# Kernel optimization log

Hardware: AMD Instinct MI355X
Metric: run time of the kernel (lower is better)

## Reference

```python
import jax, jax.numpy as jnp
import numpy as np

QLEN, B, D = 1024, 4, 512
H, DH = 8, 64
MEM, DMLP = 1024, 2048
KLEN = MEM + QLEN
EPS = 1e-5


def layer_norm(x, g, b):
    mu = jnp.mean(x, axis=-1, keepdims=True)
    var = jnp.var(x, axis=-1, keepdims=True)
    return (x - mu) * jax.lax.rsqrt(var + EPS) * g + b


def rel_shift(x):
    # x: [qlen, klen, b, h] -- Transformer-XL relative shift trick
    q, k, b, h = x.shape
    zp = jnp.zeros((q, 1, b, h), dtype=x.dtype)
    x = jnp.concatenate([zp, x], axis=1)          # [q, k+1, b, h]
    x = x.reshape(k + 1, q, b, h)[1:]             # drop first row
    return x.reshape(q, k, b, h)


def setup_inputs() -> dict:
    key = jax.random.key(0)
    ks = jax.random.split(key, 12)
    s = 0.02
    inp = {
        "inputs": jax.random.normal(ks[0], (QLEN, B, D), jnp.float32),
        "r": jax.random.normal(ks[1], (KLEN, D), jnp.float32),
        "u": jax.random.normal(ks[2], (H, DH), jnp.float32) * s,
        "v": jax.random.normal(ks[3], (H, DH), jnp.float32) * s,
        "mem": jax.random.normal(ks[4], (MEM, B, D), jnp.float32),
        # causal mask: query i (global pos MEM+i) cannot attend key j > MEM+i
        "attn_mask": jnp.arange(KLEN)[None, :] > (jnp.arange(QLEN)[:, None] + MEM),
        "Wqkv": jax.random.normal(ks[5], (3 * D, D), jnp.float32) * s,
        "Wr": jax.random.normal(ks[6], (D, D), jnp.float32) * s,
        "Wo": jax.random.normal(ks[7], (D, D), jnp.float32) * s,
        "ln1_g": jnp.ones((D,), jnp.float32),
        "ln1_b": jnp.zeros((D,), jnp.float32),
        "mlp_w1": jax.random.normal(ks[8], (DMLP, D), jnp.float32) * s,
        "mlp_b1": jnp.zeros((DMLP,), jnp.float32),
        "mlp_w2": jax.random.normal(ks[9], (D, DMLP), jnp.float32) * s,
        "mlp_b2": jnp.zeros((D,), jnp.float32),
        "ln2_g": jnp.ones((D,), jnp.float32),
        "ln2_b": jnp.zeros((D,), jnp.float32),
    }
    return inp


def reference(inputs, r, u, v, mem, attn_mask, Wqkv, Wr, Wo,
              ln1_g, ln1_b, mlp_w1, mlp_b1, mlp_w2, mlp_b2, ln2_g, ln2_b):
    qlen, b, d = inputs.shape
    cat = jnp.concatenate([mem, inputs], axis=0)          # [klen, b, d]
    klen = cat.shape[0]
    qkv = cat @ Wqkv.T                                    # [klen, b, 3d]
    q, k, w_v = jnp.split(qkv, 3, axis=-1)
    q = q[-qlen:].reshape(qlen, b, H, DH)
    k = k.reshape(klen, b, H, DH)
    w_v = w_v.reshape(klen, b, H, DH)
    rk = (r @ Wr.T).reshape(klen, H, DH)                  # [klen, h, dh]

    AC = jnp.einsum('ibhd,jbhd->ijbh', q + u, k)          # content term
    BD = jnp.einsum('ibhd,jhd->ijbh', q + v, rk)          # position term
    BD = rel_shift(BD)
    scale = 1.0 / np.sqrt(DH)
    score = (AC + BD) * scale                             # [q, k, b, h]
    score = jnp.where(attn_mask[:, :, None, None], jnp.float32(-1e30), score)
    prob = jax.nn.softmax(score, axis=1)
    attn = jnp.einsum('ijbh,jbhd->ibhd', prob, w_v).reshape(qlen, b, d)
    attn_out = attn @ Wo.T

    y = layer_norm(inputs + attn_out, ln1_g, ln1_b)
    h = jax.nn.relu(y @ mlp_w1.T + mlp_b1)
    z = h @ mlp_w2.T + mlp_b2
    out = layer_norm(y + z, ln2_g, ln2_b)
    return out, prob
```

## Files before the change

kernel.cpp:

```cpp
#include <hip/hip_runtime.h>
#include <math.h>

#define QL 1024
#define BSZ 4
#define DM 512
#define NH 8
#define DHH 64
#define MEML 1024
#define KL 2048
#define DMLP 2048

typedef __attribute__((ext_vector_type(8))) short bf16x8;
typedef __attribute__((ext_vector_type(4))) float f32x4;

#define MFMA16(A, B, C) __builtin_amdgcn_mfma_f32_16x16x32_bf16((A), (B), (C), 0, 0, 0)
#define SWZB(r, cb) (((r) << 7) + ((cb) ^ (((r) & 7) << 4)))
#define RINGB(r, c) (((r) << 9) + ((((c) << 2)) ^ (((r) & 7) << 4)))
#define CVT2(dst, lo, hi) \
  asm("v_cvt_pk_bf16_f32 %0, %1, %2" : "=v"(dst) : "v"(lo), "v"(hi))

__global__ __launch_bounds__(256)
void precvt_kernel(const float* __restrict__ src, unsigned short* __restrict__ hi,
                   unsigned short* __restrict__ lo, int n4) {
  const int i = blockIdx.x * 256 + threadIdx.x;
  if (i >= n4) return;
  const float4 a = ((const float4*)src)[i];
  uint2 h, l;
  CVT2(h.x, a.x, a.y); CVT2(h.y, a.z, a.w);
  float4 res;
  res.x = a.x - __uint_as_float(h.x << 16);
  res.y = a.y - __uint_as_float(h.x & 0xffff0000u);
  res.z = a.z - __uint_as_float(h.y << 16);
  res.w = a.w - __uint_as_float(h.y & 0xffff0000u);
  CVT2(l.x, res.x, res.y); CVT2(l.y, res.z, res.w);
  ((uint2*)hi)[i] = h;
  ((uint2*)lo)[i] = l;
}

template<int BM, bool APRE, bool BIAS, bool RELU>
__global__ __launch_bounds__(256)
void gemm_nt_mfma(const float* __restrict__ A0, const float* __restrict__ A1, int M0,
                  const unsigned short* __restrict__ AhiG, const unsigned short* __restrict__ AloG,
                  const unsigned short* __restrict__ WhiG, const unsigned short* __restrict__ WloG,
                  const float* __restrict__ bias,
                  float* __restrict__ C, int M, int N, int K) {
  constexpr int MR = 4;
  constexpr int NR = (BM == 128) ? 4 : 2;
  constexpr int AU = BM / 16;
  __shared__ __align__(16) unsigned short Ahi[BM * 64];
  __shared__ __align__(16) unsigned short Alo[BM * 64];
  __shared__ __align__(16) unsigned short Bhi[128 * 64];
  __shared__ __align__(16) unsigned short Blo[128 * 64];

  const int t = threadIdx.x;
  const int w = t >> 6;
  const int lane = t & 63;
  const int lq = lane & 15;
  const int lg = lane >> 4;
  const int row0 = blockIdx.y * BM, col0 = blockIdx.x * 128;
  const int wrow0 = (BM == 128) ? (w >> 1) * 64 : 0;
  const int wcol0 = (BM == 128) ? (w & 1) * 64 : w * 32;

  float4 paf[AU];
  uint2 pah[AU], pal[AU];
  uint2 pwh[8], pwl[8];

  auto loadAB = [&](int k0) {
    #pragma unroll
    for (int it = 0; it < AU; ++it) {
      const int idx = it * 256 + t;
      const int row = idx >> 4, c4 = (idx & 15) * 4;
      if (APRE) {
        const size_t off = (size_t)(row0 + row) * K + k0 + c4;
        pah[it] = *(const uint2*)(AhiG + off);
        pal[it] = *(const uint2*)(AloG + off);
      } else {
        const int grow = row0 + row;
        const float* src = (grow < M0) ? (A0 + (size_t)grow * K)
                                       : (A1 + (size_t)(grow - M0) * K);
        paf[it] = *(const float4*)(src + k0 + c4);
      }
    }
    #pragma unroll
    for (int it = 0; it < 8; ++it) {
      const int idx = it * 256 + t;
      const int row = idx >> 4, c4 = (idx & 15) * 4;
      const size_t off = (size_t)(col0 + row) * K + k0 + c4;
      pwh[it] = *(const uint2*)(WhiG + off);
      pwl[it] = *(const uint2*)(WloG + off);
    }
  };

  f32x4 acc[MR][NR];
  #pragma unroll
  for (int m = 0; m < MR; ++m)
    #pragma unroll
    for (int n = 0; n < NR; ++n)
      acc[m][n] = (f32x4){0.f, 0.f, 0.f, 0.f};

  loadAB(0);
  for (int k0 = 0; k0 < K; k0 += 64) {
    __syncthreads();
    #pragma unroll
    for (int it = 0; it < AU; ++it) {
      const int idx = it * 256 + t;
      const int row = idx >> 4, cb = (idx & 15) * 8;
      uint2 hi, lo;
      if (APRE) {
        hi = pah[it]; lo = pal[it];
      } else {
        const float4 a = paf[it];
        CVT2(hi.x, a.x, a.y); CVT2(hi.y, a.z, a.w);
        float4 res;
        res.x = a.x - __uint_as_float(hi.x << 16);
        res.y = a.y - __uint_as_float(hi.x & 0xffff0000u);
        res.z = a.z - __uint_as_float(hi.y << 16);
        res.w = a.w - __uint_as_float(hi.y & 0xffff0000u);
        CVT2(lo.x, res.x, res.y); CVT2(lo.y, res.z, res.w);
      }
      *(uint2*)((char*)Ahi + SWZB(row, cb)) = hi;
      *(uint2*)((char*)Alo + SWZB(row, cb)) = lo;
    }
    #pragma unroll
    for (int it = 0; it < 8; ++it) {
      const int idx = it * 256 + t;
      const int row = idx >> 4, cb = (idx & 15) * 8;
      *(uint2*)((char*)Bhi + SWZB(row, cb)) = pwh[it];
      *(uint2*)((char*)Blo + SWZB(row, cb)) = pwl[it];
    }
    __syncthreads();
    if (k0 + 64 < K) loadAB(k0 + 64);
    #pragma unroll
    for (int ks = 0; ks < 2; ++ks) {
      bf16x8 ah[MR], al[MR], bh[NR], bl[NR];
      #pragma unroll
      for (int m = 0; m < MR; ++m) {
        ah[m] = *(const bf16x8*)((const char*)Ahi + SWZB(wrow0 + m * 16 + lq, ks * 64 + lg * 16));
        al[m] = *(const bf16x8*)((const char*)Alo + SWZB(wrow0 + m * 16 + lq, ks * 64 + lg * 16));
      }
      #pragma unroll
      for (int n = 0; n < NR; ++n) {
        bh[n] = *(const bf16x8*)((const char*)Bhi + SWZB(wcol0 + n * 16 + lq, ks * 64 + lg * 16));
        bl[n] = *(const bf16x8*)((const char*)Blo + SWZB(wcol0 + n * 16 + lq, ks * 64 + lg * 16));
      }
      #pragma unroll
      for (int m = 0; m < MR; ++m)
        #pragma unroll
        for (int n = 0; n < NR; ++n) {
          acc[m][n] = MFMA16(ah[m], bh[n], acc[m][n]);
          acc[m][n] = MFMA16(ah[m], bl[n], acc[m][n]);
          acc[m][n] = MFMA16(al[m], bh[n], acc[m][n]);
        }
    }
  }
  #pragma unroll
  for (int n = 0; n < NR; ++n) {
    const int col = col0 + wcol0 + n * 16 + lq;
    const float bv = BIAS ? bias[col] : 0.f;
    #pragma unroll
    for (int m = 0; m < MR; ++m) {
      #pragma unroll
      for (int rg = 0; rg < 4; ++rg) {
        const int row = row0 + wrow0 + m * 16 + lg * 4 + rg;
        float vv = acc[m][n][rg] + bv;
        if (RELU) vv = fmaxf(vv, 0.f);
        C[(size_t)row * N + col] = vv;
      }
    }
  }
}

__global__ __launch_bounds__(256)
void ukvr_kernel(const float* __restrict__ QKV, const float* __restrict__ RK,
                 const float* __restrict__ u, const float* __restrict__ v,
                 float* __restrict__ UK, float* __restrict__ VR) {
  const int id = blockIdx.x * 256 + threadIdx.x;
  if (id < 65536) {
    const int bh = id >> 11, j = id & 2047;
    const int b = bh >> 3, h = bh & 7;
    const float* kp = QKV + ((size_t)j * 4 + b) * 1536 + 512 + h * 64;
    const float* up = u + h * 64;
    float s = 0.f;
    #pragma unroll
    for (int d = 0; d < 64; ++d) s += up[d] * kp[d];
    UK[id] = s;
  } else if (id < 65536 + 16384) {
    const int e = id - 65536;
    const int h = e >> 11, jr = e & 2047;
    const float* rp = RK + (size_t)jr * 512 + h * 64;
    const float* vp = v + h * 64;
    float s = 0.f;
    #pragma unroll
    for (int d = 0; d < 64; ++d) s += vp[d] * rp[d];
    VR[e] = s;
  }
}

__global__ __launch_bounds__(256)
void attn2_kernel(const float* __restrict__ QKV, const float* __restrict__ RK,
                  const float* __restrict__ UK, const float* __restrict__ VR,
                  unsigned short* __restrict__ P, float* __restrict__ INV,
                  float* __restrict__ ATTN) {
  const int b = blockIdx.y;
  const int h = blockIdx.z;
  const int i0 = (((h >> 2) & 1) ? (15 - (int)blockIdx.x) : (int)blockIdx.x) * 64;
  const int t = threadIdx.x;
  const int w = t >> 6;
  const int lane = t & 63;
  const int lq = lane & 15;
  const int lg = lane >> 4;

  __shared__ __align__(16) unsigned short Ks[4096];
  __shared__ __align__(16) unsigned short Rs[4096];
  __shared__ __align__(16) unsigned short Vt[4096];
  __shared__ __align__(16) unsigned short Es[4096];
  __shared__ __align__(16) float Ring[8192];
  __shared__ float uks[64];

  {
    const int jr0p = 960 - i0;
    #pragma unroll
    for (int it = 0; it < 4; ++it) {
      const int idx = it * 256 + t;
      const int row = idx >> 4, c4 = (idx & 15) * 4;
      const float4 q4 = *(const float4*)(QKV + ((size_t)(MEML + i0 + row) * 4 + b) * 1536 + h * 64 + c4);
      uint2 qp; CVT2(qp.x, q4.x, q4.y); CVT2(qp.y, q4.z, q4.w);
      *(uint2*)((char*)Es + SWZB(row, c4 * 2)) = qp;
      const float4 r4 = *(const float4*)(RK + (size_t)(jr0p + row) * 512 + h * 64 + c4);
      uint2 rp; CVT2(rp.x, r4.x, r4.y); CVT2(rp.y, r4.z, r4.w);
      *(uint2*)((char*)Rs + SWZB(row, c4 * 2)) = rp;
    }
  }
  __syncthreads();

  float4 pk[4], pr[4], pvv[4];
  float puk;
  auto load_tile = [&](int n) {
    const int j0 = n * 64;
    const int jr0 = j0 - i0 + 1024;
    #pragma unroll
    for (int it = 0; it < 4; ++it) {
      const int idx = it * 256 + t;
      const int row = idx >> 4, c4 = (idx & 15) * 4;
      pk[it] = *(const float4*)(QKV + ((size_t)(j0 + row) * 4 + b) * 1536 + 512 + h * 64 + c4);
      const int jr = jr0 + row;
      float4 r4 = make_float4(0.f, 0.f, 0.f, 0.f);
      if (jr < 2048) r4 = *(const float4*)(RK + (size_t)jr * 512 + h * 64 + c4);
      pr[it] = r4;
    }
    const int jb = (t >> 4) * 4, db = (t & 15) * 4;
    const float* vb = QKV + ((size_t)(j0 + jb) * 4 + b) * 1536 + 1024 + h * 64 + db;
    pvv[0] = *(const float4*)(vb);
    pvv[1] = *(const float4*)(vb + 6144);
    pvv[2] = *(const float4*)(vb + 12288);
    pvv[3] = *(const float4*)(vb + 18432);
    puk = (t < 64) ? UK[(size_t)(b * 8 + h) * 2048 + j0 + t] : 0.f;
  };
  load_tile(0);

  const bf16x8 qf0 = *(const bf16x8*)((const char*)Es + SWZB(w * 16 + lq, lg * 16));
  const bf16x8 qf1 = *(const bf16x8*)((const char*)Es + SWZB(w * 16 + lq, 64 + lg * 16));

  {
    f32x4 zero = {0.f, 0.f, 0.f, 0.f};
    f32x4 bd[4];
    #pragma unroll
    for (int nj = 0; nj < 4; ++nj) bd[nj] = zero;
    #pragma unroll
    for (int nj = 0; nj < 4; ++nj) {
      const bf16x8 rf0 = *(const bf16x8*)((const char*)Rs + SWZB(nj * 16 + lq, lg * 16));
      const bf16x8 rf1 = *(const bf16x8*)((const char*)Rs + SWZB(nj * 16 + lq, 64 + lg * 16));
      bd[nj] = MFMA16(qf0, rf0, bd[nj]);
      bd[nj] = MFMA16(qf1, rf1, bd[nj]);
    }
    const int jr0p = 960 - i0;
    #pragma unroll
    for (int nj = 0; nj < 4; ++nj) {
      const int jrl = nj * 16 + lq;
      const float vrv = VR[h * 2048 + jr0p + jrl];
      #pragma unroll
      for (int rg = 0; rg < 4; ++rg) {
        const int il = w * 16 + lg * 4 + rg;
        *(float*)((char*)Ring + RINGB(il, 64 + jrl)) = bd[nj][rg] + vrv;
      }
    }
  }

  f32x4 pv[4];
  {
    f32x4 zero = {0.f, 0.f, 0.f, 0.f};
    #pragma unroll
    for (int nd = 0; nd < 4; ++nd) pv[nd] = zero;
  }
  float rs[4] = {0.f, 0.f, 0.f, 0.f};

  const int ntiles = i0 / 64 + 17;
  for (int n = 0; n < ntiles; ++n) {
    const int j0 = n * 64;
    const int jr0 = j0 - i0 + 1024;
    __syncthreads();
    #pragma unroll
    for (int it = 0; it < 4; ++it) {
      const int idx = it * 256 + t;
      const int row = idx >> 4, c4 = (idx & 15) * 4;
      uint2 kp; CVT2(kp.x, pk[it].x, pk[it].y); CVT2(kp.y, pk[it].z, pk[it].w);
      *(uint2*)((char*)Ks + SWZB(row, c4 * 2)) = kp;
      uint2 rp; CVT2(rp.x, pr[it].x, pr[it].y); CVT2(rp.y, pr[it].z, pr[it].w);
      *(uint2*)((char*)Rs + SWZB(row, c4 * 2)) = rp;
    }
    {
      const int jb = (t >> 4) * 4, db = (t & 15) * 4;
      uint2 wv;
      CVT2(wv.x, pvv[0].x, pvv[1].x); CVT2(wv.y, pvv[2].x, pvv[3].x);
      *(uint2*)((char*)Vt + SWZB(db + 0, jb * 2)) = wv;
      CVT2(wv.x, pvv[0].y, pvv[1].y); CVT2(wv.y, pvv[2].y, pvv[3].y);
      *(uint2*)((char*)Vt + SWZB(db + 1, jb * 2)) = wv;
      CVT2(wv.x, pvv[0].z, pvv[1].z); CVT2(wv.y, pvv[2].z, pvv[3].z);
      *(uint2*)((char*)Vt + SWZB(db + 2, jb * 2)) = wv;
      CVT2(wv.x, pvv[0].w, pvv[1].w); CVT2(wv.y, pvv[2].w, pvv[3].w);
      *(uint2*)((char*)Vt + SWZB(db + 3, jb * 2)) = wv;
    }
    if (t < 64) uks[t] = puk;
    __syncthreads();
    if (n + 1 < ntiles) load_tile(n + 1);
    f32x4 acc[4], bdn[4];
    {
      f32x4 zero = {0.f, 0.f, 0.f, 0.f};
      #pragma unroll
      for (int nj = 0; nj < 4; ++nj) { acc[nj] = zero; bdn[nj] = zero; }
    }
    #pragma unroll
    for (int nj = 0; nj < 4; ++nj) {
      const bf16x8 kf0 = *(const bf16x8*)((const char*)Ks + SWZB(nj * 16 + lq, lg * 16));
      const bf16x8 rf0 = *(const bf16x8*)((const char*)Rs + SWZB(nj * 16 + lq, lg * 16));
      acc[nj] = MFMA16(qf0, kf0, acc[nj]);
      bdn[nj] = MFMA16(qf0, rf0, bdn[nj]);
      const bf16x8 kf1 = *(const bf16x8*)((const char*)Ks + SWZB(nj * 16 + lq, 64 + lg * 16));
      const bf16x8 rf1 = *(const bf16x8*)((const char*)Rs + SWZB(nj * 16 + lq, 64 + lg * 16));
      acc[nj] = MFMA16(qf1, kf1, acc[nj]);
      bdn[nj] = MFMA16(qf1, rf1, bdn[nj]);
    }
    const int base_cur = (n & 1) * 64;
    const int base_prev = 64 - base_cur;
    #pragma unroll
    for (int nj = 0; nj < 4; ++nj) {
      const int jrl = nj * 16 + lq;
      const int jrg = jr0 + jrl;
      const float vrv = (jrg < 2048) ? VR[h * 2048 + jrg] : 0.f;
      #pragma unroll
      for (int rg = 0; rg < 4; ++rg) {
        const int il = w * 16 + lg * 4 + rg;
        *(float*)((char*)Ring + RINGB(il, base_cur + jrl)) = bdn[nj][rg] + vrv;
      }
    }
    #pragma unroll
    for (int njp = 0; njp < 2; ++njp) {
      #pragma unroll
      for (int rg = 0; rg < 4; ++rg) {
        const int il = w * 16 + lg * 4 + rg;
        const int ig = i0 + il;
        float ee[2];
        #pragma unroll
        for (int q2 = 0; q2 < 2; ++q2) {
          const int nj = njp * 2 + q2;
          const int jl = nj * 16 + lq;
          const int jr_rel = jl - il + 63;
          const float ringv = (jr_rel < 64)
              ? *(const float*)((const char*)Ring + RINGB(il, base_prev + jr_rel))
              : *(const float*)((const char*)Ring + RINGB(il, base_cur + jr_rel - 64));
          const float s = 0.125f * (acc[nj][rg] + ringv + uks[jl]);
          const float e = (j0 + jl > ig + MEML) ? 0.f : __expf(s);
          rs[rg] += e;
          ee[q2] = e;
        }
        unsigned int pk2; CVT2(pk2, ee[0], ee[1]);
        const int jlA = (njp * 2) * 16 + lq;
        *(unsigned short*)((char*)Es + SWZB(il, jlA * 2)) = (unsigned short)(pk2 & 0xffffu);
        *(unsigned short*)((char*)Es + SWZB(il, (jlA + 16) * 2)) = (unsigned short)(pk2 >> 16);
      }
    }
    {
      const bf16x8 pf0 = *(const bf16x8*)((const char*)Es + SWZB(w * 16 + lq, lg * 16));
      const bf16x8 pf1 = *(const bf16x8*)((const char*)Es + SWZB(w * 16 + lq, 64 + lg * 16));
      #pragma unroll
      for (int nd = 0; nd < 4; ++nd) {
        const bf16x8 vf0 = *(const bf16x8*)((const char*)Vt + SWZB(nd * 16 + lq, lg * 16));
        const bf16x8 vf1 = *(const bf16x8*)((const char*)Vt + SWZB(nd * 16 + lq, 64 + lg * 16));
        pv[nd] = MFMA16(pf0, vf0, pv[nd]);
        pv[nd] = MFMA16(pf1, vf1, pv[nd]);
      }
    }
    __syncthreads();
    #pragma unroll
    for (int it = 0; it < 2; ++it) {
      const int c = it * 256 + t;
      const int row = c >> 3, c16 = c & 7;
      const uint4 val = *(const uint4*)((const char*)Es + SWZB(row, c16 * 16));
      *(uint4*)(P + ((size_t)(b * 8 + h) * 1024 + i0 + row) * 2048 + j0 + c16 * 8) = val;
    }
  }

  #pragma unroll
  for (int rg = 0; rg < 4; ++rg) {
    #pragma unroll
    for (int m = 1; m < 16; m <<= 1) rs[rg] += __shfl_xor(rs[rg], m, 64);
  }
  float inv[4];
  #pragma unroll
  for (int rg = 0; rg < 4; ++rg) inv[rg] = 1.0f / rs[rg];
  if (lq == 0) {
    #pragma unroll
    for (int rg = 0; rg < 4; ++rg)
      INV[(size_t)(b * 8 + h) * 1024 + i0 + w * 16 + lg * 4 + rg] = inv[rg];
  }
  #pragma unroll
  for (int nd = 0; nd < 4; ++nd) {
    #pragma unroll
    for (int rg = 0; rg < 4; ++rg) {
      ATTN[((size_t)(i0 + w * 16 + lg * 4 + rg) * 4 + b) * 512 + h * 64 + nd * 16 + lq] =
          pv[nd][rg] * inv[rg];
    }
  }
}

__global__ __launch_bounds__(256)
void ptrans_kernel(const unsigned short* __restrict__ P, const float* __restrict__ INV,
                   float* __restrict__ prob) {
  const int i  = blockIdx.x;
  const int j0 = blockIdx.y * 64;
  const int t  = threadIdx.x;
  __shared__ float tile[32][65];
  __shared__ float invs[32];
  const bool valid = j0 <= (i & ~63) + MEML;
  if (t < 32) invs[t] = INV[(size_t)t * 1024 + i];
  if (valid) {
    const int bh = t >> 3, part = t & 7;
    const uint4 raw = *(const uint4*)(P + ((size_t)bh * 1024 + i) * 2048 + j0 + part * 8);
    const unsigned int w[4] = {raw.x, raw.y, raw.z, raw.w};
    #pragma unroll
    for (int k = 0; k < 4; ++k) {
      tile[bh][part*8 + 2*k]     = __uint_as_float(w[k] << 16);
      tile[bh][part*8 + 2*k + 1] = __uint_as_float(w[k] & 0xffff0000u);
    }
  }
  __syncthreads();
  #pragma unroll
  for (int it = 0; it < 8; ++it) {
    const int idx = it * 256 + t;
    const int jl = idx >> 5, bh = idx & 31;
    const float val = valid ? tile[bh][jl] * invs[bh] : 0.f;
    prob[((size_t)i * 2048 + j0 + jl) * 32 + bh] = val;
  }
}

__global__ __launch_bounds__(256)
void ln_res_kernel(const float* __restrict__ xa, const float* __restrict__ xb,
                   const float* __restrict__ g, const float* __restrict__ bb,
                   float* __restrict__ y) {
  const int rrow = blockIdx.x;
  const int t = threadIdx.x;
  const size_t base = (size_t)rrow * DM;
  __shared__ float red[256];
  const float a0 = xa[base + t]       + xb[base + t];
  const float a1 = xa[base + t + 256] + xb[base + t + 256];
  red[t] = a0 + a1; __syncthreads();
  for (int s = 128; s > 0; s >>= 1) { if (t < s) red[t] += red[t+s]; __syncthreads(); }
  const float mu = red[0] * (1.0f/512.0f);
  __syncthreads();
  red[t] = a0*a0 + a1*a1; __syncthreads();
  for (int s = 128; s > 0; s >>= 1) { if (t < s) red[t] += red[t+s]; __syncthreads(); }
  const float var = red[0] * (1.0f/512.0f) - mu*mu;
  const float w = rsqrtf(var + 1e-5f);
  y[base + t]       = (a0 - mu) * w * g[t]       + bb[t];
  y[base + t + 256] = (a1 - mu) * w * g[t + 256] + bb[t + 256];
}

extern "C" void kernel_launch(void* const* d_in, const int* in_sizes, int n_in,
                              void* d_out, int out_size, void* d_ws, size_t ws_size,
                              hipStream_t stream) {
  const float* inputs = (const float*)d_in[0];
  const float* r      = (const float*)d_in[1];
  const float* u      = (const float*)d_in[2];
  const float* v      = (const float*)d_in[3];
  const float* mem    = (const float*)d_in[4];
  const float* Wqkv   = (const float*)d_in[6];
  const float* Wr     = (const float*)d_in[7];
  const float* Wo     = (const float*)d_in[8];
  const float* ln1g   = (const float*)d_in[9];
  const float* ln1b   = (const float*)d_in[10];
  const float* w1     = (const float*)d_in[11];
  const float* b1     = (const float*)d_in[12];
  const float* w2     = (const float*)d_in[13];
  const float* b2     = (const float*)d_in[14];
  const float* ln2g   = (const float*)d_in[15];
  const float* ln2b   = (const float*)d_in[16];

  float* out  = (float*)d_out;
  float* prob = out + (size_t)QL*BSZ*DM;

  float* ws   = (float*)d_ws;
  unsigned short* P = (unsigned short*)ws;
  float* QKV  = ws + 33554432;
  float* RK   = QKV + 12582912;
  float* ATTN = RK + 1048576;
  float* AO   = ATTN + 2097152;
  float* Y    = AO + 2097152;
  float* UK   = Y + 2097152;
  float* VR   = UK + 65536;
  float* INV  = VR + 16384;
  float* HM   = ws;
  float* Z    = ws + 8388608;

  unsigned short* CAThi  = (unsigned short*)ws;
  unsigned short* CATlo  = CAThi + 4194304;
  unsigned short* Rhi    = CATlo + 4194304;
  unsigned short* Rlo    = Rhi + 1048576;
  unsigned short* Wqkvhi = Rlo + 1048576;
  unsigned short* Wqkvlo = Wqkvhi + 786432;
  unsigned short* Wrhi   = Wqkvlo + 786432;
  unsigned short* Wrlo   = Wrhi + 262144;
  unsigned short* Wohi = (unsigned short*)(ws + 10485760);
  unsigned short* Wolo = Wohi + 262144;
  unsigned short* w1hi = Wolo + 262144;
  unsigned short* w1lo = w1hi + 1048576;
  unsigned short* w2hi = w1lo + 1048576;
  unsigned short* w2lo = w2hi + 1048576;

  const dim3 blk256(256);

  precvt_kernel<<<dim3(2048), blk256, 0, stream>>>(mem, CAThi, CATlo, 524288);
  precvt_kernel<<<dim3(2048), blk256, 0, stream>>>(inputs, CAThi + 2097152, CATlo + 2097152, 524288);
  precvt_kernel<<<dim3(1024), blk256, 0, stream>>>(r, Rhi, Rlo, 262144);
  precvt_kernel<<<dim3(768),  blk256, 0, stream>>>(Wqkv, Wqkvhi, Wqkvlo, 196608);
  precvt_kernel<<<dim3(256),  blk256, 0, stream>>>(Wr, Wrhi, Wrlo, 65536);

  gemm_nt_mfma<128,true,false,false><<<dim3(12, 64), blk256, 0, stream>>>(
      nullptr, nullptr, 0, CAThi, CATlo, Wqkvhi, Wqkvlo, nullptr, QKV, 8192, 1536, 512);
  gemm_nt_mfma<64,true,false,false><<<dim3(4, 32), blk256, 0, stream>>>(
      nullptr, nullptr, 0, Rhi, Rlo, Wrhi, Wrlo, nullptr, RK, 2048, 512, 512);
  ukvr_kernel<<<dim3(320), blk256, 0, stream>>>(QKV, RK, u, v, UK, VR);
  attn2_kernel<<<dim3(16, BSZ, NH), blk256, 0, stream>>>(QKV, RK, UK, VR, P, INV, ATTN);
  ptrans_kernel<<<dim3(1024, 32), blk256, 0, stream>>>(P, INV, prob);

  precvt_kernel<<<dim3(256),  blk256, 0, stream>>>(Wo, Wohi, Wolo, 65536);
  precvt_kernel<<<dim3(1024), blk256, 0, stream>>>(w1, w1hi, w1lo, 262144);
  precvt_kernel<<<dim3(1024), blk256, 0, stream>>>(w2, w2hi, w2lo, 262144);

  gemm_nt_mfma<64,false,false,false><<<dim3(4, 64), blk256, 0, stream>>>(
      ATTN, ATTN, 4096, nullptr, nullptr, Wohi, Wolo, nullptr, AO, 4096, 512, 512);
  ln_res_kernel<<<dim3(4096), blk256, 0, stream>>>(inputs, AO, ln1g, ln1b, Y);
  gemm_nt_mfma<128,false,true,true><<<dim3(16, 32), blk256, 0, stream>>>(
      Y, Y, 4096, nullptr, nullptr, w1hi, w1lo, b1, HM, 4096, 2048, 512);
  gemm_nt_mfma<64,false,true,false><<<dim3(4, 64), blk256, 0, stream>>>(
      HM, HM, 4096, nullptr, nullptr, w2hi, w2lo, b2, Z, 4096, 512, 2048);
  ln_res_kernel<<<dim3(4096), blk256, 0, stream>>>(Y, Z, ln2g, ln2b, out);
}
```

Measured before the change: 721.7 us.

## Pre-tile split-bf16 operands, load GEMM tiles via global_load_lds, fold u/v into queries

```diff
diff --git a/kernel.cpp b/kernel.cpp
--- a/kernel.cpp
+++ b/kernel.cpp
@@ -18,30 +18,94 @@
 #define RINGB(r, c) (((r) << 9) + ((((c) << 2)) ^ (((r) & 7) << 4)))
 #define CVT2(dst, lo, hi) \
   asm("v_cvt_pk_bf16_f32 %0, %1, %2" : "=v"(dst) : "v"(lo), "v"(hi))
+#define GLOAD_LDS(gp, lp) __builtin_amdgcn_global_load_lds( \
+    (const __attribute__((address_space(1))) void*)(gp), \
+    (__attribute__((address_space(3))) void*)(lp), 16, 0, 0)
+
+__device__ __forceinline__ void split_bf16(const float4 a, uint2& h, uint2& l) {
+  CVT2(h.x, a.x, a.y); CVT2(h.y, a.z, a.w);
+  float4 r;
+  r.x = a.x - __uint_as_float(h.x << 16);
+  r.y = a.y - __uint_as_float(h.x & 0xffff0000u);
+  r.z = a.z - __uint_as_float(h.y << 16);
+  r.w = a.w - __uint_as_float(h.y & 0xffff0000u);
+  CVT2(l.x, r.x, r.y); CVT2(l.y, r.z, r.w);
+}
+
+__device__ __forceinline__ void store_tiled(char* hiB, char* loB, int KT,
+                                            int row, int c0, uint2 h, uint2 l) {
+  const size_t off = (((size_t)(row >> 7) * KT + (c0 >> 6)) << 14)
+                   + SWZB(row & 127, (c0 & 63) * 2);
+  *(uint2*)(hiB + off) = h;
+  *(uint2*)(loB + off) = l;
+}
 
 __global__ __launch_bounds__(256)
-void precvt_kernel(const float* __restrict__ src, unsigned short* __restrict__ hi,
-                   unsigned short* __restrict__ lo, int n4) {
-  const int i = blockIdx.x * 256 + threadIdx.x;
-  if (i >= n4) return;
-  const float4 a = ((const float4*)src)[i];
-  uint2 h, l;
-  CVT2(h.x, a.x, a.y); CVT2(h.y, a.z, a.w);
-  float4 res;
-  res.x = a.x - __uint_as_float(h.x << 16);
-  res.y = a.y - __uint_as_float(h.x & 0xffff0000u);
-  res.z = a.z - __uint_as_float(h.y << 16);
-  res.w = a.w - __uint_as_float(h.y & 0xffff0000u);
-  CVT2(l.x, res.x, res.y); CVT2(l.y, res.z, res.w);
-  ((uint2*)hi)[i] = h;
-  ((uint2*)lo)[i] = l;
-}
-
-template<int BM, bool APRE, bool BIAS, bool RELU>
+void precvt_early(const float* __restrict__ mem, const float* __restrict__ inputs,
+                  const float* __restrict__ r, const float* __restrict__ Wqkv,
+                  const float* __restrict__ Wr,
+                  unsigned short* CAThi, unsigned short* CATlo,
+                  unsigned short* Rhi, unsigned short* Rlo,
+                  unsigned short* Qhi, unsigned short* Qlo,
+                  unsigned short* WrHi, unsigned short* WrLo) {
+  const int id = blockIdx.x * 256 + threadIdx.x;
+  float4 a; uint2 h, l;
+  if (id < 1048576) {
+    const int row = id >> 7, c0 = (id & 127) * 4;
+    const float* s = (row < 4096) ? mem + (size_t)row * 512
+                                  : inputs + (size_t)(row - 4096) * 512;
+    a = *(const float4*)(s + c0);
+    split_bf16(a, h, l);
+    store_tiled((char*)CAThi, (char*)CATlo, 8, row, c0, h, l);
+  } else if (id < 1310720) {
+    const int e = id - 1048576, row = e >> 7, c0 = (e & 127) * 4;
+    a = *(const float4*)(r + (size_t)row * 512 + c0);
+    split_bf16(a, h, l);
+    store_tiled((char*)Rhi, (char*)Rlo, 8, row, c0, h, l);
+  } else if (id < 1507328) {
+    const int e = id - 1310720, row = e >> 7, c0 = (e & 127) * 4;
+    a = *(const float4*)(Wqkv + (size_t)row * 512 + c0);
+    split_bf16(a, h, l);
+    store_tiled((char*)Qhi, (char*)Qlo, 8, row, c0, h, l);
+  } else if (id < 1572864) {
+    const int e = id - 1507328, row = e >> 7, c0 = (e & 127) * 4;
+    a = *(const float4*)(Wr + (size_t)row * 512 + c0);
+    split_bf16(a, h, l);
+    store_tiled((char*)WrHi, (char*)WrLo, 8, row, c0, h, l);
+  }
+}
+
+__global__ __launch_bounds__(256)
+void precvt_late(const float* __restrict__ Wo, const float* __restrict__ w1,
+                 const float* __restrict__ w2,
+                 unsigned short* WoHi, unsigned short* WoLo,
+                 unsigned short* w1Hi, unsigned short* w1Lo,
+                 unsigned short* w2Hi, unsigned short* w2Lo) {
+  const int id = blockIdx.x * 256 + threadIdx.x;
+  float4 a; uint2 h, l;
+  if (id < 65536) {
+    const int row = id >> 7, c0 = (id & 127) * 4;
+    a = *(const float4*)(Wo + (size_t)row * 512 + c0);
+    split_bf16(a, h, l);
+    store_tiled((char*)WoHi, (char*)WoLo, 8, row, c0, h, l);
+  } else if (id < 327680) {
+    const int e = id - 65536, row = e >> 7, c0 = (e & 127) * 4;
+    a = *(const float4*)(w1 + (size_t)row * 512 + c0);
+    split_bf16(a, h, l);
+    store_tiled((char*)w1Hi, (char*)w1Lo, 8, row, c0, h, l);
+  } else if (id < 589824) {
+    const int e = id - 327680, row = e >> 9, c0 = (e & 511) * 4;
+    a = *(const float4*)(w2 + (size_t)row * 2048 + c0);
+    split_bf16(a, h, l);
+    store_tiled((char*)w2Hi, (char*)w2Lo, 32, row, c0, h, l);
+  }
+}
+
+template<int BM, bool AGLDS, bool BIAS, bool RELU>
 __global__ __launch_bounds__(256)
 void gemm_nt_mfma(const float* __restrict__ A0, const float* __restrict__ A1, int M0,
-                  const unsigned short* __restrict__ AhiG, const unsigned short* __restrict__ AloG,
-                  const unsigned short* __restrict__ WhiG, const unsigned short* __restrict__ WloG,
+                  const unsigned short* __restrict__ AhiT, const unsigned short* __restrict__ AloT,
+                  const unsigned short* __restrict__ WhiT, const unsigned short* __restrict__ WloT,
                   const float* __restrict__ bias,
                   float* __restrict__ C, int M, int N, int K) {
   constexpr int MR = 4;
@@ -53,42 +117,29 @@
   __shared__ __align__(16) unsigned short Blo[128 * 64];
 
   const int t = threadIdx.x;
-  const int w = t >> 6;
-  const int lane = t & 63;
-  const int lq = lane & 15;
-  const int lg = lane >> 4;
+  const int w = t >> 6, lane = t & 63;
+  const int lq = lane & 15, lg = lane >> 4;
   const int row0 = blockIdx.y * BM, col0 = blockIdx.x * 128;
   const int wrow0 = (BM == 128) ? (w >> 1) * 64 : 0;
   const int wcol0 = (BM == 128) ? (w & 1) * 64 : w * 32;
+  const int KT = K >> 6;
+  const size_t amt = (size_t)(row0 >> 7) * KT;
+  const int asub = (row0 & 127) << 7;
+  const size_t bnt = (size_t)(col0 >> 7) * KT;
 
   float4 paf[AU];
-  uint2 pah[AU], pal[AU];
-  uint2 pwh[8], pwl[8];
-
-  auto loadAB = [&](int k0) {
-    #pragma unroll
-    for (int it = 0; it < AU; ++it) {
-      const int idx = it * 256 + t;
-      const int row = idx >> 4, c4 = (idx & 15) * 4;
-      if (APRE) {
-        const size_t off = (size_t)(row0 + row) * K + k0 + c4;
-        pah[it] = *(const uint2*)(AhiG + off);
-        pal[it] = *(const uint2*)(AloG + off);
-      } else {
+  auto loadA = [&](int k0) {
+    if (!AGLDS) {
+      #pragma unroll
+      for (int it = 0; it < AU; ++it) {
+        const int idx = it * 256 + t;
+        const int row = idx >> 4, c4 = (idx & 15) * 4;
         const int grow = row0 + row;
         const float* src = (grow < M0) ? (A0 + (size_t)grow * K)
                                        : (A1 + (size_t)(grow - M0) * K);
         paf[it] = *(const float4*)(src + k0 + c4);
       }
     }
-    #pragma unroll
-    for (int it = 0; it < 8; ++it) {
-      const int idx = it * 256 + t;
-      const int row = idx >> 4, c4 = (idx & 15) * 4;
-      const size_t off = (size_t)(col0 + row) * K + k0 + c4;
-      pwh[it] = *(const uint2*)(WhiG + off);
-      pwl[it] = *(const uint2*)(WloG + off);
-    }
   };
 
   f32x4 acc[MR][NR];
@@ -98,38 +149,41 @@
     for (int n = 0; n < NR; ++n)
       acc[m][n] = (f32x4){0.f, 0.f, 0.f, 0.f};
 
-  loadAB(0);
-  for (int k0 = 0; k0 < K; k0 += 64) {
+  loadA(0);
+  for (int kt = 0; kt < KT; ++kt) {
     __syncthreads();
-    #pragma unroll
-    for (int it = 0; it < AU; ++it) {
-      const int idx = it * 256 + t;
-      const int row = idx >> 4, cb = (idx & 15) * 8;
-      uint2 hi, lo;
-      if (APRE) {
-        hi = pah[it]; lo = pal[it];
-      } else {
-        const float4 a = paf[it];
-        CVT2(hi.x, a.x, a.y); CVT2(hi.y, a.z, a.w);
-        float4 res;
-        res.x = a.x - __uint_as_float(hi.x << 16);
-        res.y = a.y - __uint_as_float(hi.x & 0xffff0000u);
-        res.z = a.z - __uint_as_float(hi.y << 16);
-        res.w = a.w - __uint_as_float(hi.y & 0xffff0000u);
-        CVT2(lo.x, res.x, res.y); CVT2(lo.y, res.z, res.w);
-      }
-      *(uint2*)((char*)Ahi + SWZB(row, cb)) = hi;
-      *(uint2*)((char*)Alo + SWZB(row, cb)) = lo;
-    }
-    #pragma unroll
-    for (int it = 0; it < 8; ++it) {
-      const int idx = it * 256 + t;
-      const int row = idx >> 4, cb = (idx & 15) * 8;
-      *(uint2*)((char*)Bhi + SWZB(row, cb)) = pwh[it];
-      *(uint2*)((char*)Blo + SWZB(row, cb)) = pwl[it];
+    {
+      const char* gbh = (const char*)WhiT + ((bnt + kt) << 14);
+      const char* gbl = (const char*)WloT + ((bnt + kt) << 14);
+      #pragma unroll
+      for (int i = 0; i < 4; ++i) {
+        const int off = (w * 4 + i) * 1024;
+        GLOAD_LDS(gbh + off + lane * 16, (char*)Bhi + off);
+        GLOAD_LDS(gbl + off + lane * 16, (char*)Blo + off);
+      }
+    }
+    if (AGLDS) {
+      const char* gah = (const char*)AhiT + ((amt + kt) << 14) + asub;
+      const char* gal = (const char*)AloT + ((amt + kt) << 14) + asub;
+      #pragma unroll
+      for (int i = 0; i < BM / 32; ++i) {
+        const int off = (w * (BM / 32) + i) * 1024;
+        GLOAD_LDS(gah + off + lane * 16, (char*)Ahi + off);
+        GLOAD_LDS(gal + off + lane * 16, (char*)Alo + off);
+      }
+    } else {
+      #pragma unroll
+      for (int it = 0; it < AU; ++it) {
+        const int idx = it * 256 + t;
+        const int row = idx >> 4, cb = (idx & 15) * 8;
+        uint2 hi, lo;
+        split_bf16(paf[it], hi, lo);
+        *(uint2*)((char*)Ahi + SWZB(row, cb)) = hi;
+        *(uint2*)((char*)Alo + SWZB(row, cb)) = lo;
+      }
     }
     __syncthreads();
-    if (k0 + 64 < K) loadAB(k0 + 64);
+    if (!AGLDS && kt + 1 < KT) loadA((kt + 1) * 64);
     #pragma unroll
     for (int ks = 0; ks < 2; ++ks) {
       bf16x8 ah[MR], al[MR], bh[NR], bl[NR];
@@ -171,34 +225,8 @@
 }
 
 __global__ __launch_bounds__(256)
-void ukvr_kernel(const float* __restrict__ QKV, const float* __restrict__ RK,
-                 const float* __restrict__ u, const float* __restrict__ v,
-                 float* __restrict__ UK, float* __restrict__ VR) {
-  const int id = blockIdx.x * 256 + threadIdx.x;
-  if (id < 65536) {
-    const int bh = id >> 11, j = id & 2047;
-    const int b = bh >> 3, h = bh & 7;
-    const float* kp = QKV + ((size_t)j * 4 + b) * 1536 + 512 + h * 64;
-    const float* up = u + h * 64;
-    float s = 0.f;
-    #pragma unroll
-    for (int d = 0; d < 64; ++d) s += up[d] * kp[d];
-    UK[id] = s;
-  } else if (id < 65536 + 16384) {
-    const int e = id - 65536;
-    const int h = e >> 11, jr = e & 2047;
-    const float* rp = RK + (size_t)jr * 512 + h * 64;
-    const float* vp = v + h * 64;
-    float s = 0.f;
-    #pragma unroll
-    for (int d = 0; d < 64; ++d) s += vp[d] * rp[d];
-    VR[e] = s;
-  }
-}
-
-__global__ __launch_bounds__(256)
 void attn2_kernel(const float* __restrict__ QKV, const float* __restrict__ RK,
-                  const float* __restrict__ UK, const float* __restrict__ VR,
+                  const float* __restrict__ u, const float* __restrict__ v,
                   unsigned short* __restrict__ P, float* __restrict__ INV,
                   float* __restrict__ ATTN) {
   const int b = blockIdx.y;
@@ -215,7 +243,6 @@
   __shared__ __align__(16) unsigned short Vt[4096];
   __shared__ __align__(16) unsigned short Es[4096];
   __shared__ __align__(16) float Ring[8192];
-  __shared__ float uks[64];
 
   {
     const int jr0p = 960 - i0;
@@ -224,17 +251,21 @@
       const int idx = it * 256 + t;
       const int row = idx >> 4, c4 = (idx & 15) * 4;
       const float4 q4 = *(const float4*)(QKV + ((size_t)(MEML + i0 + row) * 4 + b) * 1536 + h * 64 + c4);
-      uint2 qp; CVT2(qp.x, q4.x, q4.y); CVT2(qp.y, q4.z, q4.w);
+      const float4 u4 = *(const float4*)(u + h * 64 + c4);
+      const float4 v4 = *(const float4*)(v + h * 64 + c4);
+      uint2 qp;
+      CVT2(qp.x, q4.x + u4.x, q4.y + u4.y); CVT2(qp.y, q4.z + u4.z, q4.w + u4.w);
       *(uint2*)((char*)Es + SWZB(row, c4 * 2)) = qp;
+      CVT2(qp.x, q4.x + v4.x, q4.y + v4.y); CVT2(qp.y, q4.z + v4.z, q4.w + v4.w);
+      *(uint2*)((char*)Ks + SWZB(row, c4 * 2)) = qp;
       const float4 r4 = *(const float4*)(RK + (size_t)(jr0p + row) * 512 + h * 64 + c4);
-      uint2 rp; CVT2(rp.x, r4.x, r4.y); CVT2(rp.y, r4.z, r4.w);
-      *(uint2*)((char*)Rs + SWZB(row, c4 * 2)) = rp;
+      CVT2(qp.x, r4.x, r4.y); CVT2(qp.y, r4.z, r4.w);
+      *(uint2*)((char*)Rs + SWZB(row, c4 * 2)) = qp;
     }
   }
   __syncthreads();
 
   float4 pk[4], pr[4], pvv[4];
-  float puk;
   auto load_tile = [&](int n) {
     const int j0 = n * 64;
     const int jr0 = j0 - i0 + 1024;
@@ -254,50 +285,44 @@
     pvv[1] = *(const float4*)(vb + 6144);
     pvv[2] = *(const float4*)(vb + 12288);
     pvv[3] = *(const float4*)(vb + 18432);
-    puk = (t < 64) ? UK[(size_t)(b * 8 + h) * 2048 + j0 + t] : 0.f;
   };
   load_tile(0);
 
-  const bf16x8 qf0 = *(const bf16x8*)((const char*)Es + SWZB(w * 16 + lq, lg * 16));
-  const bf16x8 qf1 = *(const bf16x8*)((const char*)Es + SWZB(w * 16 + lq, 64 + lg * 16));
+  const bf16x8 qu0 = *(const bf16x8*)((const char*)Es + SWZB(w * 16 + lq, lg * 16));
+  const bf16x8 qu1 = *(const bf16x8*)((const char*)Es + SWZB(w * 16 + lq, 64 + lg * 16));
+  const bf16x8 qv0 = *(const bf16x8*)((const char*)Ks + SWZB(w * 16 + lq, lg * 16));
+  const bf16x8 qv1 = *(const bf16x8*)((const char*)Ks + SWZB(w * 16 + lq, 64 + lg * 16));
 
   {
-    f32x4 zero = {0.f, 0.f, 0.f, 0.f};
     f32x4 bd[4];
     #pragma unroll
-    for (int nj = 0; nj < 4; ++nj) bd[nj] = zero;
+    for (int nj = 0; nj < 4; ++nj) bd[nj] = (f32x4){0.f, 0.f, 0.f, 0.f};
     #pragma unroll
     for (int nj = 0; nj < 4; ++nj) {
       const bf16x8 rf0 = *(const bf16x8*)((const char*)Rs + SWZB(nj * 16 + lq, lg * 16));
       const bf16x8 rf1 = *(const bf16x8*)((const char*)Rs + SWZB(nj * 16 + lq, 64 + lg * 16));
-      bd[nj] = MFMA16(qf0, rf0, bd[nj]);
-      bd[nj] = MFMA16(qf1, rf1, bd[nj]);
-    }
-    const int jr0p = 960 - i0;
+      bd[nj] = MFMA16(qv0, rf0, bd[nj]);
+      bd[nj] = MFMA16(qv1, rf1, bd[nj]);
+    }
     #pragma unroll
     for (int nj = 0; nj < 4; ++nj) {
       const int jrl = nj * 16 + lq;
-      const float vrv = VR[h * 2048 + jr0p + jrl];
       #pragma unroll
       for (int rg = 0; rg < 4; ++rg) {
         const int il = w * 16 + lg * 4 + rg;
-        *(float*)((char*)Ring + RINGB(il, 64 + jrl)) = bd[nj][rg] + vrv;
+        *(float*)((char*)Ring + RINGB(il, 64 + jrl)) = bd[nj][rg];
       }
     }
   }
 
   f32x4 pv[4];
-  {
-    f32x4 zero = {0.f, 0.f, 0.f, 0.f};
-    #pragma unroll
-    for (int nd = 0; nd < 4; ++nd) pv[nd] = zero;
-  }
+  #pragma unroll
+  for (int nd = 0; nd < 4; ++nd) pv[nd] = (f32x4){0.f, 0.f, 0.f, 0.f};
   float rs[4] = {0.f, 0.f, 0.f, 0.f};
 
   const int ntiles = i0 / 64 + 17;
   for (int n = 0; n < ntiles; ++n) {
     const int j0 = n * 64;
-    const int jr0 = j0 - i0 + 1024;
     __syncthreads();
     #pragma unroll
     for (int it = 0; it < 4; ++it) {
@@ -320,37 +345,34 @@
       CVT2(wv.x, pvv[0].w, pvv[1].w); CVT2(wv.y, pvv[2].w, pvv[3].w);
       *(uint2*)((char*)Vt + SWZB(db + 3, jb * 2)) = wv;
     }
-    if (t < 64) uks[t] = puk;
     __syncthreads();
     if (n + 1 < ntiles) load_tile(n + 1);
     f32x4 acc[4], bdn[4];
-    {
-      f32x4 zero = {0.f, 0.f, 0.f, 0.f};
-      #pragma unroll
-      for (int nj = 0; nj < 4; ++nj) { acc[nj] = zero; bdn[nj] = zero; }
+    #pragma unroll
+    for (int nj = 0; nj < 4; ++nj) {
+      acc[nj] = (f32x4){0.f, 0.f, 0.f, 0.f};
+      bdn[nj] = (f32x4){0.f, 0.f, 0.f, 0.f};
     }
     #pragma unroll
     for (int nj = 0; nj < 4; ++nj) {
       const bf16x8 kf0 = *(const bf16x8*)((const char*)Ks + SWZB(nj * 16 + lq, lg * 16));
       const bf16x8 rf0 = *(const bf16x8*)((const char*)Rs + SWZB(nj * 16 + lq, lg * 16));
-      acc[nj] = MFMA16(qf0, kf0, acc[nj]);
-      bdn[nj] = MFMA16(qf0, rf0, bdn[nj]);
+      acc[nj] = MFMA16(qu0, kf0, acc[nj]);
+      bdn[nj] = MFMA16(qv0, rf0, bdn[nj]);
       const bf16x8 kf1 = *(const bf16x8*)((const char*)Ks + SWZB(nj * 16 + lq, 64 + lg * 16));
       const bf16x8 rf1 = *(const bf16x8*)((const char*)Rs + SWZB(nj * 16 + lq, 64 + lg * 16));
-      acc[nj] = MFMA16(qf1, kf1, acc[nj]);
-      bdn[nj] = MFMA16(qf1, rf1, bdn[nj]);
+      acc[nj] = MFMA16(qu1, kf1, acc[nj]);
+      bdn[nj] = MFMA16(qv1, rf1, bdn[nj]);
     }
     const int base_cur = (n & 1) * 64;
     const int base_prev = 64 - base_cur;
     #pragma unroll
     for (int nj = 0; nj < 4; ++nj) {
       const int jrl = nj * 16 + lq;
-      const int jrg = jr0 + jrl;
-      const float vrv = (jrg < 2048) ? VR[h * 2048 + jrg] : 0.f;
       #pragma unroll
       for (int rg = 0; rg < 4; ++rg) {
         const int il = w * 16 + lg * 4 + rg;
-        *(float*)((char*)Ring + RINGB(il, base_cur + jrl)) = bdn[nj][rg] + vrv;
+        *(float*)((char*)Ring + RINGB(il, base_cur + jrl)) = bdn[nj][rg];
       }
     }
     #pragma unroll
@@ -368,7 +390,7 @@
           const float ringv = (jr_rel < 64)
               ? *(const float*)((const char*)Ring + RINGB(il, base_prev + jr_rel))
               : *(const float*)((const char*)Ring + RINGB(il, base_cur + jr_rel - 64));
-          const float s = 0.125f * (acc[nj][rg] + ringv + uks[jl]);
+          const float s = 0.125f * (acc[nj][rg] + ringv);
           const float e = (j0 + jl > ig + MEML) ? 0.f : __expf(s);
           rs[rg] += e;
           ee[q2] = e;
@@ -390,11 +412,11 @@
         pv[nd] = MFMA16(pf1, vf1, pv[nd]);
       }
     }
-    __syncthreads();
     #pragma unroll
     for (int it = 0; it < 2; ++it) {
-      const int c = it * 256 + t;
-      const int row = c >> 3, c16 = c & 7;
+      const int lin = it * 64 + lane;
+      const int rr = lin >> 3, c16 = lin & 7;
+      const int row = w * 16 + rr;
       const uint4 val = *(const uint4*)((const char*)Es + SWZB(row, c16 * 16));
       *(uint4*)(P + ((size_t)(b * 8 + h) * 1024 + i0 + row) * 2048 + j0 + c16 * 8) = val;
     }
@@ -505,53 +527,46 @@
   float* ATTN = RK + 1048576;
   float* AO   = ATTN + 2097152;
   float* Y    = AO + 2097152;
-  float* UK   = Y + 2097152;
-  float* VR   = UK + 65536;
-  float* INV  = VR + 16384;
+  float* INV  = Y + 2097152;
   float* HM   = ws;
   float* Z    = ws + 8388608;
 
-  unsigned short* CAThi  = (unsigned short*)ws;
-  unsigned short* CATlo  = CAThi + 4194304;
-  unsigned short* Rhi    = CATlo + 4194304;
-  unsigned short* Rlo    = Rhi + 1048576;
-  unsigned short* Wqkvhi = Rlo + 1048576;
-  unsigned short* Wqkvlo = Wqkvhi + 786432;
-  unsigned short* Wrhi   = Wqkvlo + 786432;
-  unsigned short* Wrlo   = Wrhi + 262144;
-  unsigned short* Wohi = (unsigned short*)(ws + 10485760);
-  unsigned short* Wolo = Wohi + 262144;
-  unsigned short* w1hi = Wolo + 262144;
-  unsigned short* w1lo = w1hi + 1048576;
-  unsigned short* w2hi = w1lo + 1048576;
-  unsigned short* w2lo = w2hi + 1048576;
+  unsigned short* CAThiT = (unsigned short*)ws;
+  unsigned short* CATloT = CAThiT + 4194304;
+  unsigned short* RhiT   = CATloT + 4194304;
+  unsigned short* RloT   = RhiT + 1048576;
+  unsigned short* WqhiT  = RloT + 1048576;
+  unsigned short* WqloT  = WqhiT + 786432;
+  unsigned short* WrhiT  = WqloT + 786432;
+  unsigned short* WrloT  = WrhiT + 262144;
+  unsigned short* WohiT = (unsigned short*)(ws + 53510144);
+  unsigned short* WoloT = WohiT + 262144;
+  unsigned short* w1hiT = WoloT + 262144;
+  unsigned short* w1loT = w1hiT + 1048576;
+  unsigned short* w2hiT = w1loT + 1048576;
+  unsigned short* w2loT = w2hiT + 1048576;
 
   const dim3 blk256(256);
 
-  precvt_kernel<<<dim3(2048), blk256, 0, stream>>>(mem, CAThi, CATlo, 524288);
-  precvt_kernel<<<dim3(2048), blk256, 0, stream>>>(inputs, CAThi + 2097152, CATlo + 2097152, 524288);
-  precvt_kernel<<<dim3(1024), blk256, 0, stream>>>(r, Rhi, Rlo, 262144);
-  precvt_kernel<<<dim3(768),  blk256, 0, stream>>>(Wqkv, Wqkvhi, Wqkvlo, 196608);
-  precvt_kernel<<<dim3(256),  blk256, 0, stream>>>(Wr, Wrhi, Wrlo, 65536);
+  precvt_early<<<dim3(6144), blk256, 0, stream>>>(
+      mem, inputs, r, Wqkv, Wr,
+      CAThiT, CATloT, RhiT, RloT, WqhiT, WqloT, WrhiT, WrloT);
+  precvt_late<<<dim3(2304), blk256, 0, stream>>>(
+      Wo, w1, w2, WohiT, WoloT, w1hiT, w1loT, w2hiT, w2loT);
 
   gemm_nt_mfma<128,true,false,false><<<dim3(12, 64), blk256, 0, stream>>>(
-      nullptr, nullptr, 0, CAThi, CATlo, Wqkvhi, Wqkvlo, nullptr, QKV, 8192, 1536, 512);
+      nullptr, nullptr, 0, CAThiT, CATloT, WqhiT, WqloT, nullptr, QKV, 8192, 1536, 512);
   gemm_nt_mfma<64,true,false,false><<<dim3(4, 32), blk256, 0, stream>>>(
-      nullptr, nullptr, 0, Rhi, Rlo, Wrhi, Wrlo, nullptr, RK, 2048, 512, 512);
-  ukvr_kernel<<<dim3(320), blk256, 0, stream>>>(QKV, RK, u, v, UK, VR);
-  attn2_kernel<<<dim3(16, BSZ, NH), blk256, 0, stream>>>(QKV, RK, UK, VR, P, INV, ATTN);
+      nullptr, nullptr, 0, RhiT, RloT, WrhiT, WrloT, nullptr, RK, 2048, 512, 512);
+  attn2_kernel<<<dim3(16, BSZ, NH), blk256, 0, stream>>>(QKV, RK, u, v, P, INV, ATTN);
   ptrans_kernel<<<dim3(1024, 32), blk256, 0, stream>>>(P, INV, prob);
 
-  precvt_kernel<<<dim3(256),  blk256, 0, stream>>>(Wo, Wohi, Wolo, 65536);
-  precvt_kernel<<<dim3(1024), blk256, 0, stream>>>(w1, w1hi, w1lo, 262144);
-  precvt_kernel<<<dim3(1024), blk256, 0, stream>>>(w2, w2hi, w2lo, 262144);
-
   gemm_nt_mfma<64,false,false,false><<<dim3(4, 64), blk256, 0, stream>>>(
-      ATTN, ATTN, 4096, nullptr, nullptr, Wohi, Wolo, nullptr, AO, 4096, 512, 512);
+      ATTN, ATTN, 4096, nullptr, nullptr, WohiT, WoloT, nullptr, AO, 4096, 512, 512);
   ln_res_kernel<<<dim3(4096), blk256, 0, stream>>>(inputs, AO, ln1g, ln1b, Y);
   gemm_nt_mfma<128,false,true,true><<<dim3(16, 32), blk256, 0, stream>>>(
-      Y, Y, 4096, nullptr, nullptr, w1hi, w1lo, b1, HM, 4096, 2048, 512);
+      Y, Y, 4096, nullptr, nullptr, w1hiT, w1loT, b1, HM, 4096, 2048, 512);
   gemm_nt_mfma<64,false,true,false><<<dim3(4, 64), blk256, 0, stream>>>(
-      HM, HM, 4096, nullptr, nullptr, w2hi, w2lo, b2, Z, 4096, 512, 2048);
+      HM, HM, 4096, nullptr, nullptr, w2hiT, w2loT, b2, Z, 4096, 512, 2048);
   ln_res_kernel<<<dim3(4096), blk256, 0, stream>>>(Y, Z, ln2g, ln2b, out);
 }
```

After: 643.6 us. 10.8% less time.
